# Performance work log

Hardware: AMD Instinct MI355X
Metric: run time of the kernel (lower is better)

## Reference

```python
import sys
import jax, jax.numpy as jnp
import numpy as np

sys.setrecursionlimit(100000)

MARGIN = 200.0
SAME_MARGIN = 0.0
REL_MARGIN = MARGIN - SAME_MARGIN  # margin - same_margin


def km_algorithm(mp):
    """Faithful numpy port of the repo's recursive Kuhn-Munkres (host-side,
    exactly mirroring the original CPU round-trip). mp: (n, n) float64.
    Returns transport plan T with T[link[y], y] = 1/n for matched pairs."""
    n = mp.shape[0]
    link = np.full(n, -1, dtype=np.int64)
    lx = mp.max(axis=1).astype(np.float64).copy()
    ly = np.zeros(n, dtype=np.float64)
    st = {}

    def dfs(x):
        st['visx'][x] = True
        for y in range(n):
            if st['visy'][y]:
                continue
            tmp = lx[x] + ly[y] - mp[x, y]
            if abs(tmp) < 1e-5:
                st['visy'][y] = True
                if link[y] == -1 or dfs(link[y]):
                    link[y] = x
                    return True
            elif st['sla'][y] + 1e-5 > tmp:
                st['sla'][y] = tmp
        return False

    for x in range(n):
        st['sla'] = np.full(n, 1e10, dtype=np.float64)
        while True:
            st['visx'] = np.zeros(n, dtype=bool)
            st['visy'] = np.zeros(n, dtype=bool)
            if dfs(x):
                break
            d = st['sla'][~st['visy']].min()
            lx[st['visx']] -= d
            ly[st['visy']] += d
            st['sla'][~st['visy']] -= d
    T = np.zeros((n, n), dtype=np.float64)
    for i in range(n):
        if link[i] != -1:
            T[link[i], i] = 1.0 / n
    return T


def sim_label(l1, l2):
    # (n, n) float: 1 where labels equal
    return (l1[:, None] == l2[None, :]).astype(jnp.float32)


def ground_metric(f1, f2, sim):
    # pairwise squared euclidean distances: ||a||^2 - 2 a.b + ||b||^2
    sq1 = jnp.sum(f1 * f1, axis=1)[:, None]
    sq2 = jnp.sum(f2 * f2, axis=1)[None, :]
    d2 = sq1 - 2.0 * (f1 @ f2.T) + sq2
    hinge_gm = jnp.maximum(0.0, SAME_MARGIN + REL_MARGIN - d2)   # negative pairs
    same_gm = jnp.maximum(0.0, d2 - SAME_MARGIN)                 # positive pairs
    return sim * same_gm + (1.0 - sim) * hinge_gm                # mode='both'


def setup_inputs() -> dict:
    key = jax.random.key(0)
    k1, k2, k3, k4 = jax.random.split(key, 4)
    n, d = 128, 8192
    return {
        "inputs_batch1": jax.random.normal(k1, (n, d), dtype=jnp.float32),
        "inputs_batch2": jax.random.normal(k2, (n, d), dtype=jnp.float32),
        "targets_batch1": jax.random.randint(k3, (n,), 0, 16, dtype=jnp.int64) if jax.config.jax_enable_x64 else jax.random.randint(k3, (n,), 0, 16).astype(jnp.int32),
        "targets_batch2": jax.random.randint(k4, (n,), 0, 16, dtype=jnp.int64) if jax.config.jax_enable_x64 else jax.random.randint(k4, (n,), 0, 16).astype(jnp.int32),
    }


def reference(inputs_batch1, inputs_batch2, targets_batch1, targets_batch2):
    sim = sim_label(targets_batch1, targets_batch2)
    GM = ground_metric(inputs_batch1, inputs_batch2, sim)
    # host round-trip for KM assignment, as in the original module
    T = km_algorithm(np.asarray(jax.device_get(GM), dtype=np.float64))
    T = jnp.asarray(T, dtype=jnp.float32)
    loss = jnp.sum(GM * T)
    return loss
```

## Files before the change

kernel.cpp:

```cpp
#include <hip/hip_runtime.h>

#define N 128
#define DIM 8192
#define NN (N * N)
#define ZSPLIT 64
#define NW 16
#define GSTRIDE 130
#define NSTR 65

__device__ __forceinline__ void wave_fence() {
    __threadfence_block();
    __builtin_amdgcn_wave_barrier();
}
__device__ __forceinline__ double embed_key(double v, int j) {
    long long b = __double_as_longlong(v);
    return __longlong_as_double((b & ~127LL) | (long long)j);
}

__global__ __launch_bounds__(256) void d2_partial(const float* __restrict__ A,
                                                  const float* __restrict__ B,
                                                  float* __restrict__ d2p,
                                                  float* __restrict__ sqAp,
                                                  float* __restrict__ sqBp) {
    __shared__ float As[32][68];
    __shared__ float Bk[64][36];
    const int tid = threadIdx.x;
    const int bi = blockIdx.x, bj = blockIdx.y, bz = blockIdx.z;
    const int tx = tid & 15, ty = tid >> 4;
    const int row0 = bi * 32, col0 = bj * 32;
    const int kbase = bz * 128;

    if (bj == 0) {
        const int r = tid >> 3, seg = tid & 7;
        const float* pa = &A[(row0 + r) * DIM + kbase + seg * 16];
        float s = 0.f;
        #pragma unroll
        for (int u = 0; u < 4; ++u) {
            float4 v = *(const float4*)&pa[u * 4];
            s = fmaf(v.x, v.x, fmaf(v.y, v.y, fmaf(v.z, v.z, fmaf(v.w, v.w, s))));
        }
        #pragma unroll
        for (int o = 1; o < 8; o <<= 1) s += __shfl_xor(s, o, 64);
        if (seg == 0) sqAp[bz * 128 + row0 + r] = s;
    }
    if (bi == 0) {
        const int r = tid >> 3, seg = tid & 7;
        const float* pb = &B[(col0 + r) * DIM + kbase + seg * 16];
        float s = 0.f;
        #pragma unroll
        for (int u = 0; u < 4; ++u) {
            float4 v = *(const float4*)&pb[u * 4];
            s = fmaf(v.x, v.x, fmaf(v.y, v.y, fmaf(v.z, v.z, fmaf(v.w, v.w, s))));
        }
        #pragma unroll
        for (int o = 1; o < 8; o <<= 1) s += __shfl_xor(s, o, 64);
        if (seg == 0) sqBp[bz * 128 + col0 + r] = s;
    }

    float a00 = 0.f, a01 = 0.f, a10 = 0.f, a11 = 0.f;
    for (int it = 0; it < 2; ++it) {
        const int k0 = kbase + it * 64;
        __syncthreads();
        #pragma unroll
        for (int s = 0; s < 2; ++s) {
            int e = tid + s * 256;
            int r = e >> 4, q = e & 15;
            *(float4*)&As[r][q * 4] = *(const float4*)&A[(row0 + r) * DIM + k0 + q * 4];
        }
        #pragma unroll
        for (int s = 0; s < 2; ++s) {
            int r = tid & 31;
            int kq = (tid >> 5) + s * 8;
            float4 b4 = *(const float4*)&B[(col0 + r) * DIM + k0 + kq * 4];
            Bk[kq * 4 + 0][r] = b4.x;
            Bk[kq * 4 + 1][r] = b4.y;
            Bk[kq * 4 + 2][r] = b4.z;
            Bk[kq * 4 + 3][r] = b4.w;
        }
        __syncthreads();
        #pragma unroll
        for (int kk = 0; kk < 64; kk += 4) {
            float x0[4], x1[4];
            *(float4*)x0 = *(const float4*)&As[2 * ty][kk];
            *(float4*)x1 = *(const float4*)&As[2 * ty + 1][kk];
            float y[4][2];
            #pragma unroll
            for (int q = 0; q < 4; ++q)
                *(float2*)y[q] = *(const float2*)&Bk[kk + q][2 * tx];
            #pragma unroll
            for (int q = 0; q < 4; ++q) {
                a00 = fmaf(x0[q], y[q][0], a00);
                a01 = fmaf(x0[q], y[q][1], a01);
                a10 = fmaf(x1[q], y[q][0], a10);
                a11 = fmaf(x1[q], y[q][1], a11);
            }
        }
    }
    const int o0 = (row0 + 2 * ty) * N + col0 + 2 * tx;
    float* dst = d2p + bz * NN;
    *(float2*)&dst[o0]     = make_float2(a00, a01);
    *(float2*)&dst[o0 + N] = make_float2(a10, a11);
}

__global__ __launch_bounds__(256) void reduce_gm(const float* __restrict__ d2p,
                                                 const float* __restrict__ sqAp,
                                                 const float* __restrict__ sqBp,
                                                 const int* __restrict__ t1,
                                                 const int* __restrict__ t2,
                                                 float* __restrict__ gm,
                                                 int* __restrict__ flagarr) {
    __shared__ float sqA_l[128], sqB_l[128];
    __shared__ int bf;
    const int tid = threadIdx.x;
    if (tid == 0) bf = 0;
    {
        const int c = tid & 127;
        const float* src = (tid < 128) ? (sqBp + c) : (sqAp + c);
        float t0 = 0.f, t1_ = 0.f, t2_ = 0.f, t3 = 0.f, t4 = 0.f, t5 = 0.f, t6 = 0.f, t7 = 0.f;
        #pragma unroll
        for (int z = 0; z < ZSPLIT; z += 8) {
            t0 += src[(z + 0) * 128]; t1_ += src[(z + 1) * 128];
            t2_ += src[(z + 2) * 128]; t3 += src[(z + 3) * 128];
            t4 += src[(z + 4) * 128]; t5 += src[(z + 5) * 128];
            t6 += src[(z + 6) * 128]; t7 += src[(z + 7) * 128];
        }
        float s = ((t0 + t1_) + (t2_ + t3)) + ((t4 + t5) + (t6 + t7));
        if (tid < 128) sqB_l[c] = s; else sqA_l[c] = s;
    }
    const int o = blockIdx.x * 256 + tid;
    float s0 = 0.f, s1 = 0.f, s2 = 0.f, s3 = 0.f, s4 = 0.f, s5 = 0.f, s6 = 0.f, s7 = 0.f;
    const float* p = d2p + o;
    #pragma unroll
    for (int z = 0; z < ZSPLIT; z += 8) {
        s0 += p[(z + 0) * NN]; s1 += p[(z + 1) * NN];
        s2 += p[(z + 2) * NN]; s3 += p[(z + 3) * NN];
        s4 += p[(z + 4) * NN]; s5 += p[(z + 5) * NN];
        s6 += p[(z + 6) * NN]; s7 += p[(z + 7) * NN];
    }
    float dot = ((s0 + s1) + (s2 + s3)) + ((s4 + s5) + (s6 + s7));
    __syncthreads();
    const int i = o >> 7, j = o & 127;
    const float s = sqA_l[i] + sqB_l[j] - 2.f * dot;
    const int l1 = t1[i], l2 = t2[j];
    const bool same = (l1 == l2);
    float g = same ? fmaxf(s, 0.f) : fmaxf(200.f - s, 0.f);
    gm[o] = g;
    bool bad = (!same && g > 0.f) || l1 < 0 || l1 > 63 || l2 < 0 || l2 > 63;
    unsigned long long m = __ballot(bad);
    if ((tid & 63) == 0 && m) atomicOr(&bf, 1);
    __syncthreads();
    if (tid == 0) flagarr[blockIdx.x] = bf;
}

__global__ __launch_bounds__(64) void solve_classes(const float* __restrict__ gm,
                                                    const int* __restrict__ flagarr,
                                                    const int* __restrict__ t1,
                                                    const int* __restrict__ t2,
                                                    double* __restrict__ cls_val) {
    __shared__ float ncls[64 * NSTR];
    __shared__ int rowl[64], coll[64];
    __shared__ int rcnt[64], ccnt[64];
    __shared__ int tasks[64];
    __shared__ int clm[64];

    const int lane = threadIdx.x;
    const int l1a = t1[lane] & 63, l1b = t1[lane + 64] & 63;
    const int l2a = t2[lane] & 63, l2b = t2[lane + 64] & 63;
    const int fl  = flagarr[lane];
    rcnt[lane] = 0; ccnt[lane] = 0;
    __syncthreads();
    atomicAdd(&rcnt[l1a], 1); atomicAdd(&rcnt[l1b], 1);
    atomicAdd(&ccnt[l2a], 1); atomicAdd(&ccnt[l2b], 1);
    __syncthreads();
    const bool flag = (__ballot(fl != 0) != 0ull);
    int ntasks;
    {
        int R = rcnt[lane], C = ccnt[lane];
        bool small = (!flag) && (R > 0) && (C > 0) && (R <= 64) && (C <= 64);
        unsigned long long ms = __ballot(small);
        if (small) tasks[__popcll(ms & ((1ull << lane) - 1))] = lane;
        ntasks = (int)__popcll(ms);
    }
    __syncthreads();
    if ((int)blockIdx.x >= ntasks) {
        if (lane == 0) cls_val[blockIdx.x] = 0.0;
        return;
    }
    const int c = tasks[blockIdx.x];

    const unsigned long long mlt = (1ull << lane) - 1;
    unsigned long long b1 = __ballot(l1a == c);
    unsigned long long b2 = __ballot(l1b == c);
    if (l1a == c) rowl[__popcll(b1 & mlt)] = lane;
    if (l1b == c) rowl[__popcll(b1) + __popcll(b2 & mlt)] = lane + 64;
    const int Rn = (int)(__popcll(b1) + __popcll(b2));
    unsigned long long c1 = __ballot(l2a == c);
    unsigned long long c2 = __ballot(l2b == c);
    if (l2a == c) coll[__popcll(c1 & mlt)] = lane;
    if (l2b == c) coll[__popcll(c1) + __popcll(c2 & mlt)] = lane + 64;
    const int Cn = (int)(__popcll(c1) + __popcll(c2));
    __syncthreads();

    const bool T  = (Rn > Cn);
    const int n_  = T ? Cn : Rn;
    const int m_  = T ? Rn : Cn;
    const int tot = n_ * m_;
    for (int e = lane; e < tot; e += 64) {
        int i = e / m_, j = e - i * m_;
        int gr = T ? rowl[j] : rowl[i];
        int gc = T ? coll[i] : coll[j];
        ncls[i * NSTR + j] = gm[gr * N + gc];
    }
    __syncthreads();

    const int W = (m_ <= 16) ? 16 : (m_ <= 32 ? 32 : 64);
    const bool cA = (lane < m_), rA = (lane < n_);

    double u = 0.0;
    if (rA) {
        float mx = 0.f;
        const float* row = &ncls[lane * NSTR];
        for (int j = 0; j < m_; ++j) mx = fmaxf(mx, row[j]);
        u = -(double)mx;
    }
    double v = 1e30;
    for (int i = 0; i < n_; ++i) {
        double ui = __shfl(u, i, 64);
        if (cA) v = fmin(v, -(double)ncls[i * NSTR + lane] - ui);
    }
    if (cA) clm[lane] = 0x7fffffff;
    wave_fence();
    int jc = -1;
    for (int j = 0; j < m_; ++j) {
        double vj = __shfl(v, j, 64);
        if (rA && jc < 0) {
            double s = -(double)ncls[lane * NSTR + j] - u - vj;
            if (s < 1e-7) jc = j;
        }
    }
    if (rA && jc >= 0) atomicMin(&clm[jc], lane);
    wave_fence();
    int p = -1;
    if (cA && clm[lane] != 0x7fffffff) p = clm[lane];
    bool rowm = (rA && jc >= 0 && clm[jc] == lane);

    for (int ir = 0; ir < n_; ++ir) {
        if (__shfl(rowm ? 1 : 0, ir, 64)) continue;
        double minv = 1e30, markD = -1.0, ent = -1.0;
        bool used = false; int way = -2;
        if (rA && lane == ir) ent = 0.0;
        double D = 0.0;
        int i0 = ir, jprev = -1;
        int guard = 2 * m_ + 8;
        while (guard-- > 0) {
            double ui = __shfl(u, i0, 64);
            if (cA && !used) {
                double cand = D - ui - (double)ncls[i0 * NSTR + lane] - v;
                if (cand < minv) { minv = cand; way = jprev; }
            }
            double kd = (cA && !used) ? embed_key(minv, lane) : 1e30;
            for (int o = 1; o < W; o <<= 1) kd = fmin(kd, __shfl_xor(kd, o, 64));
            long long kb = __double_as_longlong(kd);
            int j1 = (int)(kb & 127);
            double Dn = __longlong_as_double(kb & ~127LL);
            if (Dn > 1e29) break;
            D = Dn;
            int i1 = __shfl(p, j1, 64);
            if (i1 < 0) {
                int jj = j1;
                while (true) {
                    int wp = __shfl(way, jj, 64);
                    int pn = (wp < 0) ? ir : __shfl(p, wp, 64);
                    if (cA && lane == jj) p = pn;
                    if (wp < 0) break;
                    jj = wp;
                }
                if (rA && lane == ir) rowm = true;
                break;
            }
            if (cA && lane == j1) { used = true; markD = D; }
            if (rA && lane == i1) ent = D;
            jprev = j1; i0 = i1;
        }
        if (rA && ent   >= 0.0) u += D - ent;
        if (cA && markD >= 0.0) v -= D - markD;
    }

    double val = 0.0;
    if (cA && p >= 0) val = (double)ncls[p * NSTR + lane];
    #pragma unroll
    for (int o = 1; o < 64; o <<= 1) val += __shfl_xor(val, o, 64);
    if (lane == 0) cls_val[blockIdx.x] = val;
}

__global__ __launch_bounds__(1024) void finalize_kernel(const float* __restrict__ gm,
                                                        const int* __restrict__ flagarr,
                                                        const int* __restrict__ t1,
                                                        const int* __restrict__ t2,
                                                        const double* __restrict__ cls_val,
                                                        float* __restrict__ out) {
    __shared__ float gml[N * GSTRIDE];
    __shared__ int lbl1[N], lbl2[N];
    __shared__ int rowlist[N], collist[N];
    __shared__ int rcnt[64], ccnt[64], rstart[65], cstart[65], rcur[64], ccur[64];
    __shared__ int bigtasks[65];
    __shared__ int nbig_s, flag_s;
    __shared__ double ub[N + 1], vbp[N + 1], minvb[N + 1];
    __shared__ int pb[N + 1], wayb[N + 1], usedb[N + 1];
    __shared__ double redv[NW];
    __shared__ int redi[NW];
    __shared__ double big_total, small_sum;
    __shared__ int jfin_s;

    const int tid = threadIdx.x;
    if (tid < 64) { rcnt[tid] = 0; ccnt[tid] = 0; rcur[tid] = 0; ccur[tid] = 0; }
    if (tid == 0) { nbig_s = 0; flag_s = 0; big_total = 0.0; }
    if (tid < N)  { lbl1[tid] = t1[tid]; lbl2[tid] = t2[tid]; }
    __syncthreads();
    if (tid < 64 && flagarr[tid]) atomicOr(&flag_s, 1);
    if (tid < N) {
        atomicAdd(&rcnt[lbl1[tid] & 63], 1);
        atomicAdd(&ccnt[lbl2[tid] & 63], 1);
    }
    double sv = (tid < 64) ? cls_val[tid] : 0.0;
    __syncthreads();
    if (tid < 64) {
        int rs_ = rcnt[tid], cs_ = ccnt[tid];
        #pragma unroll
        for (int o = 1; o < 64; o <<= 1) {
            int tr = __shfl_up(rs_, o, 64);
            int tc = __shfl_up(cs_, o, 64);
            if (tid >= o) { rs_ += tr; cs_ += tc; }
        }
        rstart[tid + 1] = rs_;
        cstart[tid + 1] = cs_;
        if (tid == 0) { rstart[0] = 0; cstart[0] = 0; }
        if (!flag_s) {
            int R = rcnt[tid], C = ccnt[tid];
            bool big = (R > 0) && (C > 0) && ((R > 64) || (C > 64));
            unsigned long long mb = __ballot(big);
            if (big) bigtasks[__popcll(mb & ((1ull << tid) - 1))] = tid;
            if (tid == 0) nbig_s = __popcll(mb);
        } else if (tid == 0) { nbig_s = 1; bigtasks[0] = -1; }
        if (flag_s) sv = 0.0;
        #pragma unroll
        for (int o = 1; o < 64; o <<= 1) sv += __shfl_xor(sv, o, 64);
        if (tid == 0) small_sum = sv;
    }
    __syncthreads();

    const int nbig = nbig_s;
    if (nbig > 0) {
        if (tid < N) {
            int l1 = lbl1[tid] & 63;
            int p = atomicAdd(&rcur[l1], 1);
            rowlist[rstart[l1] + p] = tid;
            int l2 = lbl2[tid] & 63;
            int q = atomicAdd(&ccur[l2], 1);
            collist[cstart[l2] + q] = tid;
        }
        __syncthreads();
        #pragma unroll
        for (int pch = 0; pch < 16; ++pch) {
            int e = tid + pch * 1024;
            int i = e >> 7, j = e & 127;
            gml[i * GSTRIDE + j] = gm[rowlist[i] * N + collist[j]];
        }
        __syncthreads();

        for (int bt = 0; bt < nbig; ++bt) {
            const int c = bigtasks[bt];
            int Rn, Cn, rs, cs;
            if (c < 0) { Rn = N; Cn = N; rs = 0; cs = 0; }
            else { Rn = rcnt[c]; Cn = ccnt[c]; rs = rstart[c]; cs = cstart[c]; }
            const bool T = (Rn > Cn);
            const int n_ = T ? Cn : Rn, m_ = T ? Rn : Cn;
            const int rstep = T ? 1 : GSTRIDE;
            const int cstep = T ? GSTRIDE : 1;
            const int rb00 = T ? cs : rs * GSTRIDE;
            const int ob00 = T ? rs * GSTRIDE : cs;
            auto cost = [&](int i, int j) -> double {
                return -(double)gml[rb00 + i * rstep + ob00 + j * cstep];
            };
            for (int x = tid; x <= m_; x += 1024) { vbp[x] = 0.0; pb[x] = 0; }
            for (int x = tid; x <= n_; x += 1024) { ub[x] = 0.0; }
            __syncthreads();
            for (int i = 1; i <= n_; ++i) {
                if (tid == 0) pb[0] = i;
                for (int x = tid; x <= m_; x += 1024) { minvb[x] = 1e300; usedb[x] = 0; }
                __syncthreads();
                int j0 = 0;
                int guard = 2 * m_ + 8;
                while (guard-- > 0) {
                    if (tid == 0) usedb[j0] = 1;
                    __syncthreads();
                    const int i0 = pb[j0];
                    double dl = 1e300; int jl = 0;
                    if (tid < m_) {
                        int j = tid + 1;
                        if (!usedb[j]) {
                            double cur = cost(i0 - 1, j - 1) - ub[i0] - vbp[j];
                            if (cur < minvb[j]) { minvb[j] = cur; wayb[j] = j0; }
                            dl = minvb[j]; jl = j;
                        }
                    }
                    double rv = dl; int ri = jl;
                    #pragma unroll
                    for (int o = 32; o > 0; o >>= 1) {
                        double ov = __shfl_down(rv, o, 64);
                        int oi2 = __shfl_down(ri, o, 64);
                        if (ov < rv) { rv = ov; ri = oi2; }
                    }
                    if ((tid & 63) == 0) { redv[tid >> 6] = rv; redi[tid >> 6] = ri; }
                    __syncthreads();
                    if (tid == 0) {
                        double bd = 1e300; int bj = 0;
                        for (int q = 0; q < NW; ++q) if (redv[q] < bd) { bd = redv[q]; bj = redi[q]; }
                        redv[0] = bd; redi[0] = bj;
                    }
                    __syncthreads();
                    const double delta = redv[0];
                    const int j1 = redi[0];
                    if (tid < m_) {
                        int j = tid + 1;
                        if (usedb[j]) { ub[pb[j]] += delta; vbp[j] -= delta; }
                        else          { minvb[j] -= delta; }
                    }
                    if (tid == 0) ub[pb[0]] += delta;
                    __syncthreads();
                    j0 = j1;
                    if (pb[j0] == 0) break;
                }
                if (tid == 0) jfin_s = j0;
                __syncthreads();
                if (tid == 0) {
                    int jj = jfin_s;
                    while (jj) { int jp = wayb[jj]; pb[jj] = pb[jp]; jj = jp; }
                }
                __syncthreads();
            }
            double bl = 0.0;
            if (tid < m_) { int j = tid + 1; if (pb[j] != 0) bl = -cost(pb[j] - 1, j - 1); }
            #pragma unroll
            for (int o = 32; o > 0; o >>= 1) bl += __shfl_down(bl, o, 64);
            if ((tid & 63) == 0) redv[tid >> 6] = bl;
            __syncthreads();
            if (tid == 0) { double s = 0; for (int q = 0; q < NW; ++q) s += redv[q]; big_total += s; }
            __syncthreads();
        }
    }

    if (tid == 0) out[0] = (float)((small_sum + big_total) / (double)N);
}

extern "C" void kernel_launch(void* const* d_in, const int* in_sizes, int n_in,
                              void* d_out, int out_size, void* d_ws, size_t ws_size,
                              hipStream_t stream) {
    const float* A  = (const float*)d_in[0];
    const float* B  = (const float*)d_in[1];
    const int*   t1 = (const int*)d_in[2];
    const int*   t2 = (const int*)d_in[3];
    float* out = (float*)d_out;
    float* d2p = (float*)d_ws;
    float* gm  = d2p + ZSPLIT * NN;
    int*   flagarr = (int*)(gm + NN);
    double* cls_val = (double*)(flagarr + 64);
    float* sqAp = (float*)(cls_val + 64);
    float* sqBp = sqAp + ZSPLIT * 128;

    d2_partial<<<dim3(4, 4, ZSPLIT), 256, 0, stream>>>(A, B, d2p, sqAp, sqBp);
    reduce_gm<<<64, 256, 0, stream>>>(d2p, sqAp, sqBp, t1, t2, gm, flagarr);
    solve_classes<<<64, 64, 0, stream>>>(gm, flagarr, t1, t2, cls_val);
    finalize_kernel<<<1, 1024, 0, stream>>>(gm, flagarr, t1, t2, cls_val, out);
}
```

Before: 91.13 us.

## Fuse reduce and per-class assignment kernels, halve K-split of distance GEMM

Merges the partial-sum reduction kernel and the per-class Hungarian solver into one kernel, so one launch disappears. Each block recomputes its class's cost submatrix directly from the partial dot products instead of reading the global GM written by another block. The GEMM K-split is halved (32 slices of 256), which halves the partial buffer that must be reduced but gives fewer blocks of parallelism. The per-class solver no longer checks the global bad-pair flag, so it always solves classes and relies on the finalize kernel to handle the flagged case.

New measurement: 93.17 us. 1.02x slower.

```diff
diff --git a/kernel.cpp b/kernel.cpp
--- a/kernel.cpp
+++ b/kernel.cpp
@@ -3,7 +3,7 @@
 #define N 128
 #define DIM 8192
 #define NN (N * N)
-#define ZSPLIT 64
+#define ZSPLIT 32
 #define NW 16
 #define GSTRIDE 130
 #define NSTR 65
@@ -28,14 +28,14 @@
     const int bi = blockIdx.x, bj = blockIdx.y, bz = blockIdx.z;
     const int tx = tid & 15, ty = tid >> 4;
     const int row0 = bi * 32, col0 = bj * 32;
-    const int kbase = bz * 128;
+    const int kbase = bz * 256;
 
     if (bj == 0) {
         const int r = tid >> 3, seg = tid & 7;
-        const float* pa = &A[(row0 + r) * DIM + kbase + seg * 16];
+        const float* pa = &A[(row0 + r) * DIM + kbase + seg * 32];
         float s = 0.f;
         #pragma unroll
-        for (int u = 0; u < 4; ++u) {
+        for (int u = 0; u < 8; ++u) {
             float4 v = *(const float4*)&pa[u * 4];
             s = fmaf(v.x, v.x, fmaf(v.y, v.y, fmaf(v.z, v.z, fmaf(v.w, v.w, s))));
         }
@@ -45,10 +45,10 @@
     }
     if (bi == 0) {
         const int r = tid >> 3, seg = tid & 7;
-        const float* pb = &B[(col0 + r) * DIM + kbase + seg * 16];
+        const float* pb = &B[(col0 + r) * DIM + kbase + seg * 32];
         float s = 0.f;
         #pragma unroll
-        for (int u = 0; u < 4; ++u) {
+        for (int u = 0; u < 8; ++u) {
             float4 v = *(const float4*)&pb[u * 4];
             s = fmaf(v.x, v.x, fmaf(v.y, v.y, fmaf(v.z, v.z, fmaf(v.w, v.w, s))));
         }
@@ -58,7 +58,7 @@
     }
 
     float a00 = 0.f, a01 = 0.f, a10 = 0.f, a11 = 0.f;
-    for (int it = 0; it < 2; ++it) {
+    for (int it = 0; it < 4; ++it) {
         const int k0 = kbase + it * 64;
         __syncthreads();
         #pragma unroll
@@ -102,16 +102,23 @@
     *(float2*)&dst[o0 + N] = make_float2(a10, a11);
 }
 
-__global__ __launch_bounds__(256) void reduce_gm(const float* __restrict__ d2p,
-                                                 const float* __restrict__ sqAp,
-                                                 const float* __restrict__ sqBp,
-                                                 const int* __restrict__ t1,
-                                                 const int* __restrict__ t2,
-                                                 float* __restrict__ gm,
-                                                 int* __restrict__ flagarr) {
+__global__ __launch_bounds__(256) void reduce_solve(const float* __restrict__ d2p,
+                                                    const float* __restrict__ sqAp,
+                                                    const float* __restrict__ sqBp,
+                                                    const int* __restrict__ t1,
+                                                    const int* __restrict__ t2,
+                                                    float* __restrict__ gm,
+                                                    int* __restrict__ flagarr,
+                                                    double* __restrict__ cls_val) {
+    __shared__ float ncls[64 * NSTR];
     __shared__ float sqA_l[128], sqB_l[128];
     __shared__ int bf;
+    __shared__ int rowl[64], coll[64], rcnt[64], ccnt[64], tasks64[64], clm[64];
+    __shared__ int sT, sn, sm, shave;
+
     const int tid = threadIdx.x;
+    const int blk = blockIdx.x;
+
     if (tid == 0) bf = 0;
     {
         const int c = tid & 127;
@@ -127,170 +134,187 @@
         float s = ((t0 + t1_) + (t2_ + t3)) + ((t4 + t5) + (t6 + t7));
         if (tid < 128) sqB_l[c] = s; else sqA_l[c] = s;
     }
-    const int o = blockIdx.x * 256 + tid;
-    float s0 = 0.f, s1 = 0.f, s2 = 0.f, s3 = 0.f, s4 = 0.f, s5 = 0.f, s6 = 0.f, s7 = 0.f;
-    const float* p = d2p + o;
-    #pragma unroll
-    for (int z = 0; z < ZSPLIT; z += 8) {
-        s0 += p[(z + 0) * NN]; s1 += p[(z + 1) * NN];
-        s2 += p[(z + 2) * NN]; s3 += p[(z + 3) * NN];
-        s4 += p[(z + 4) * NN]; s5 += p[(z + 5) * NN];
-        s6 += p[(z + 6) * NN]; s7 += p[(z + 7) * NN];
-    }
-    float dot = ((s0 + s1) + (s2 + s3)) + ((s4 + s5) + (s6 + s7));
-    __syncthreads();
-    const int i = o >> 7, j = o & 127;
-    const float s = sqA_l[i] + sqB_l[j] - 2.f * dot;
-    const int l1 = t1[i], l2 = t2[j];
-    const bool same = (l1 == l2);
-    float g = same ? fmaxf(s, 0.f) : fmaxf(200.f - s, 0.f);
-    gm[o] = g;
-    bool bad = (!same && g > 0.f) || l1 < 0 || l1 > 63 || l2 < 0 || l2 > 63;
-    unsigned long long m = __ballot(bad);
-    if ((tid & 63) == 0 && m) atomicOr(&bf, 1);
-    __syncthreads();
-    if (tid == 0) flagarr[blockIdx.x] = bf;
-}
-
-__global__ __launch_bounds__(64) void solve_classes(const float* __restrict__ gm,
-                                                    const int* __restrict__ flagarr,
-                                                    const int* __restrict__ t1,
-                                                    const int* __restrict__ t2,
-                                                    double* __restrict__ cls_val) {
-    __shared__ float ncls[64 * NSTR];
-    __shared__ int rowl[64], coll[64];
-    __shared__ int rcnt[64], ccnt[64];
-    __shared__ int tasks[64];
-    __shared__ int clm[64];
-
-    const int lane = threadIdx.x;
-    const int l1a = t1[lane] & 63, l1b = t1[lane + 64] & 63;
-    const int l2a = t2[lane] & 63, l2b = t2[lane + 64] & 63;
-    const int fl  = flagarr[lane];
-    rcnt[lane] = 0; ccnt[lane] = 0;
-    __syncthreads();
-    atomicAdd(&rcnt[l1a], 1); atomicAdd(&rcnt[l1b], 1);
-    atomicAdd(&ccnt[l2a], 1); atomicAdd(&ccnt[l2b], 1);
-    __syncthreads();
-    const bool flag = (__ballot(fl != 0) != 0ull);
-    int ntasks;
+    const int o = blk * 256 + tid;
+    float dot;
     {
-        int R = rcnt[lane], C = ccnt[lane];
-        bool small = (!flag) && (R > 0) && (C > 0) && (R <= 64) && (C <= 64);
-        unsigned long long ms = __ballot(small);
-        if (small) tasks[__popcll(ms & ((1ull << lane) - 1))] = lane;
-        ntasks = (int)__popcll(ms);
-    }
-    __syncthreads();
-    if ((int)blockIdx.x >= ntasks) {
-        if (lane == 0) cls_val[blockIdx.x] = 0.0;
+        const float* p = d2p + o;
+        float s0 = 0.f, s1 = 0.f, s2 = 0.f, s3 = 0.f, s4 = 0.f, s5 = 0.f, s6 = 0.f, s7 = 0.f;
+        #pragma unroll
+        for (int z = 0; z < ZSPLIT; z += 8) {
+            s0 += p[(z + 0) * NN]; s1 += p[(z + 1) * NN];
+            s2 += p[(z + 2) * NN]; s3 += p[(z + 3) * NN];
+            s4 += p[(z + 4) * NN]; s5 += p[(z + 5) * NN];
+            s6 += p[(z + 6) * NN]; s7 += p[(z + 7) * NN];
+        }
+        dot = ((s0 + s1) + (s2 + s3)) + ((s4 + s5) + (s6 + s7));
+    }
+    __syncthreads();
+    {
+        const int i = o >> 7, j = o & 127;
+        const float s = sqA_l[i] + sqB_l[j] - 2.f * dot;
+        const int l1 = t1[i], l2 = t2[j];
+        const bool same = (l1 == l2);
+        float g = same ? fmaxf(s, 0.f) : fmaxf(200.f - s, 0.f);
+        gm[o] = g;
+        bool bad = (!same && g > 0.f) || l1 < 0 || l1 > 63 || l2 < 0 || l2 > 63;
+        unsigned long long m = __ballot(bad);
+        if ((tid & 63) == 0 && m) atomicOr(&bf, 1);
+    }
+    __syncthreads();
+    if (tid == 0) flagarr[blk] = bf;
+
+    if (tid < 64) {
+        const int lane = tid;
+        const int l1a = t1[lane] & 63, l1b = t1[lane + 64] & 63;
+        const int l2a = t2[lane] & 63, l2b = t2[lane + 64] & 63;
+        rcnt[lane] = 0; ccnt[lane] = 0;
+        wave_fence();
+        atomicAdd(&rcnt[l1a], 1); atomicAdd(&rcnt[l1b], 1);
+        atomicAdd(&ccnt[l2a], 1); atomicAdd(&ccnt[l2b], 1);
+        wave_fence();
+        int ntasks;
+        {
+            int R = rcnt[lane], C = ccnt[lane];
+            bool small = (R > 0) && (C > 0) && (R <= 64) && (C <= 64);
+            unsigned long long ms = __ballot(small);
+            if (small) tasks64[__popcll(ms & ((1ull << lane) - 1))] = lane;
+            ntasks = (int)__popcll(ms);
+        }
+        wave_fence();
+        const bool have = (blk < ntasks);
+        if (have) {
+            const int c = tasks64[blk];
+            const unsigned long long mlt = (1ull << lane) - 1;
+            unsigned long long b1 = __ballot(l1a == c);
+            unsigned long long b2 = __ballot(l1b == c);
+            if (l1a == c) rowl[__popcll(b1 & mlt)] = lane;
+            if (l1b == c) rowl[__popcll(b1) + __popcll(b2 & mlt)] = lane + 64;
+            const int Rn = (int)(__popcll(b1) + __popcll(b2));
+            unsigned long long c1 = __ballot(l2a == c);
+            unsigned long long c2 = __ballot(l2b == c);
+            if (l2a == c) coll[__popcll(c1 & mlt)] = lane;
+            if (l2b == c) coll[__popcll(c1) + __popcll(c2 & mlt)] = lane + 64;
+            const int Cn = (int)(__popcll(c1) + __popcll(c2));
+            if (lane == 0) {
+                const bool T = (Rn > Cn);
+                sT = T ? 1 : 0;
+                sn = T ? Cn : Rn;
+                sm = T ? Rn : Cn;
+            }
+        }
+        if (lane == 0) shave = have ? 1 : 0;
+    }
+    __syncthreads();
+    if (!shave) {
+        if (tid == 0) cls_val[blk] = 0.0;
         return;
     }
-    const int c = tasks[blockIdx.x];
-
-    const unsigned long long mlt = (1ull << lane) - 1;
-    unsigned long long b1 = __ballot(l1a == c);
-    unsigned long long b2 = __ballot(l1b == c);
-    if (l1a == c) rowl[__popcll(b1 & mlt)] = lane;
-    if (l1b == c) rowl[__popcll(b1) + __popcll(b2 & mlt)] = lane + 64;
-    const int Rn = (int)(__popcll(b1) + __popcll(b2));
-    unsigned long long c1 = __ballot(l2a == c);
-    unsigned long long c2 = __ballot(l2b == c);
-    if (l2a == c) coll[__popcll(c1 & mlt)] = lane;
-    if (l2b == c) coll[__popcll(c1) + __popcll(c2 & mlt)] = lane + 64;
-    const int Cn = (int)(__popcll(c1) + __popcll(c2));
-    __syncthreads();
-
-    const bool T  = (Rn > Cn);
-    const int n_  = T ? Cn : Rn;
-    const int m_  = T ? Rn : Cn;
-    const int tot = n_ * m_;
-    for (int e = lane; e < tot; e += 64) {
-        int i = e / m_, j = e - i * m_;
-        int gr = T ? rowl[j] : rowl[i];
-        int gc = T ? coll[i] : coll[j];
-        ncls[i * NSTR + j] = gm[gr * N + gc];
-    }
-    __syncthreads();
-
-    const int W = (m_ <= 16) ? 16 : (m_ <= 32 ? 32 : 64);
-    const bool cA = (lane < m_), rA = (lane < n_);
-
-    double u = 0.0;
-    if (rA) {
-        float mx = 0.f;
-        const float* row = &ncls[lane * NSTR];
-        for (int j = 0; j < m_; ++j) mx = fmaxf(mx, row[j]);
-        u = -(double)mx;
-    }
-    double v = 1e30;
-    for (int i = 0; i < n_; ++i) {
-        double ui = __shfl(u, i, 64);
-        if (cA) v = fmin(v, -(double)ncls[i * NSTR + lane] - ui);
-    }
-    if (cA) clm[lane] = 0x7fffffff;
-    wave_fence();
-    int jc = -1;
-    for (int j = 0; j < m_; ++j) {
-        double vj = __shfl(v, j, 64);
-        if (rA && jc < 0) {
-            double s = -(double)ncls[lane * NSTR + j] - u - vj;
-            if (s < 1e-7) jc = j;
-        }
-    }
-    if (rA && jc >= 0) atomicMin(&clm[jc], lane);
-    wave_fence();
-    int p = -1;
-    if (cA && clm[lane] != 0x7fffffff) p = clm[lane];
-    bool rowm = (rA && jc >= 0 && clm[jc] == lane);
-
-    for (int ir = 0; ir < n_; ++ir) {
-        if (__shfl(rowm ? 1 : 0, ir, 64)) continue;
-        double minv = 1e30, markD = -1.0, ent = -1.0;
-        bool used = false; int way = -2;
-        if (rA && lane == ir) ent = 0.0;
-        double D = 0.0;
-        int i0 = ir, jprev = -1;
-        int guard = 2 * m_ + 8;
-        while (guard-- > 0) {
-            double ui = __shfl(u, i0, 64);
-            if (cA && !used) {
-                double cand = D - ui - (double)ncls[i0 * NSTR + lane] - v;
-                if (cand < minv) { minv = cand; way = jprev; }
-            }
-            double kd = (cA && !used) ? embed_key(minv, lane) : 1e30;
-            for (int o = 1; o < W; o <<= 1) kd = fmin(kd, __shfl_xor(kd, o, 64));
-            long long kb = __double_as_longlong(kd);
-            int j1 = (int)(kb & 127);
-            double Dn = __longlong_as_double(kb & ~127LL);
-            if (Dn > 1e29) break;
-            D = Dn;
-            int i1 = __shfl(p, j1, 64);
-            if (i1 < 0) {
-                int jj = j1;
-                while (true) {
-                    int wp = __shfl(way, jj, 64);
-                    int pn = (wp < 0) ? ir : __shfl(p, wp, 64);
-                    if (cA && lane == jj) p = pn;
-                    if (wp < 0) break;
-                    jj = wp;
+
+    {
+        const int n_ = sn, m_ = sm, T = sT;
+        const int tot = n_ * m_;
+        const int sub = tid & 3;
+        for (int e = tid >> 2; e < tot; e += 64) {
+            const int i = e / m_, j = e - i * m_;
+            const int gr = T ? rowl[j] : rowl[i];
+            const int gc = T ? coll[i] : coll[j];
+            const float* p = d2p + gr * N + gc + sub * 8 * NN;
+            float q0 = 0.f, q1 = 0.f, q2 = 0.f, q3 = 0.f;
+            #pragma unroll
+            for (int z = 0; z < 8; z += 4) {
+                q0 += p[(z + 0) * NN]; q1 += p[(z + 1) * NN];
+                q2 += p[(z + 2) * NN]; q3 += p[(z + 3) * NN];
+            }
+            float s = (q0 + q1) + (q2 + q3);
+            s += __shfl_xor(s, 1, 64);
+            s += __shfl_xor(s, 2, 64);
+            if (sub == 0)
+                ncls[i * NSTR + j] = fmaxf(sqA_l[gr] + sqB_l[gc] - 2.f * s, 0.f);
+        }
+    }
+    __syncthreads();
+
+    double val = 0.0;
+    if (tid < 64) {
+        const int lane = tid;
+        const int n_ = sn, m_ = sm;
+        const int W = (m_ <= 16) ? 16 : (m_ <= 32 ? 32 : 64);
+        const bool cA = (lane < m_), rA = (lane < n_);
+
+        double u = 0.0;
+        if (rA) {
+            float mx = 0.f;
+            const float* row = &ncls[lane * NSTR];
+            for (int j = 0; j < m_; ++j) mx = fmaxf(mx, row[j]);
+            u = -(double)mx;
+        }
+        double v = 1e30;
+        for (int i = 0; i < n_; ++i) {
+            double ui = __shfl(u, i, 64);
+            if (cA) v = fmin(v, -(double)ncls[i * NSTR + lane] - ui);
+        }
+        if (cA) clm[lane] = 0x7fffffff;
+        wave_fence();
+        int jc = -1;
+        for (int j = 0; j < m_; ++j) {
+            double vj = __shfl(v, j, 64);
+            if (rA && jc < 0) {
+                double s = -(double)ncls[lane * NSTR + j] - u - vj;
+                if (s < 1e-7) jc = j;
+            }
+        }
+        if (rA && jc >= 0) atomicMin(&clm[jc], lane);
+        wave_fence();
+        int p = -1;
+        if (cA && clm[lane] != 0x7fffffff) p = clm[lane];
+        bool rowm = (rA && jc >= 0 && clm[jc] == lane);
+
+        for (int ir = 0; ir < n_; ++ir) {
+            if (__shfl(rowm ? 1 : 0, ir, 64)) continue;
+            double minv = 1e30, markD = -1.0, ent = -1.0;
+            bool used = false; int way = -2;
+            if (rA && lane == ir) ent = 0.0;
+            double D = 0.0;
+            int i0 = ir, jprev = -1;
+            int guard = 2 * m_ + 8;
+            while (guard-- > 0) {
+                double ui = __shfl(u, i0, 64);
+                if (cA && !used) {
+                    double cand = D - ui - (double)ncls[i0 * NSTR + lane] - v;
+                    if (cand < minv) { minv = cand; way = jprev; }
                 }
-                if (rA && lane == ir) rowm = true;
-                break;
-            }
-            if (cA && lane == j1) { used = true; markD = D; }
-            if (rA && lane == i1) ent = D;
-            jprev = j1; i0 = i1;
-        }
-        if (rA && ent   >= 0.0) u += D - ent;
-        if (cA && markD >= 0.0) v -= D - markD;
-    }
-
-    double val = 0.0;
-    if (cA && p >= 0) val = (double)ncls[p * NSTR + lane];
-    #pragma unroll
-    for (int o = 1; o < 64; o <<= 1) val += __shfl_xor(val, o, 64);
-    if (lane == 0) cls_val[blockIdx.x] = val;
+                double kd = (cA && !used) ? embed_key(minv, lane) : 1e30;
+                for (int oo = 1; oo < W; oo <<= 1) kd = fmin(kd, __shfl_xor(kd, oo, 64));
+                long long kb = __double_as_longlong(kd);
+                int j1 = (int)(kb & 127);
+                double Dn = __longlong_as_double(kb & ~127LL);
+                if (Dn > 1e29) break;
+                D = Dn;
+                int i1 = __shfl(p, j1, 64);
+                if (i1 < 0) {
+                    int jj = j1;
+                    while (true) {
+                        int wp = __shfl(way, jj, 64);
+                        int pn = (wp < 0) ? ir : __shfl(p, wp, 64);
+                        if (cA && lane == jj) p = pn;
+                        if (wp < 0) break;
+                        jj = wp;
+                    }
+                    if (rA && lane == ir) rowm = true;
+                    break;
+                }
+                if (cA && lane == j1) { used = true; markD = D; }
+                if (rA && lane == i1) ent = D;
+                jprev = j1; i0 = i1;
+            }
+            if (rA && ent   >= 0.0) u += D - ent;
+            if (cA && markD >= 0.0) v -= D - markD;
+        }
+        if (cA && p >= 0) val = (double)ncls[p * NSTR + lane];
+        #pragma unroll
+        for (int oo = 1; oo < 64; oo <<= 1) val += __shfl_xor(val, oo, 64);
+    }
+    if (tid == 0) cls_val[blk] = val;
 }
 
 __global__ __launch_bounds__(1024) void finalize_kernel(const float* __restrict__ gm,
@@ -469,7 +493,6 @@
     float* sqBp = sqAp + ZSPLIT * 128;
 
     d2_partial<<<dim3(4, 4, ZSPLIT), 256, 0, stream>>>(A, B, d2p, sqAp, sqBp);
-    reduce_gm<<<64, 256, 0, stream>>>(d2p, sqAp, sqBp, t1, t2, gm, flagarr);
-    solve_classes<<<64, 64, 0, stream>>>(gm, flagarr, t1, t2, cls_val);
+    reduce_solve<<<64, 256, 0, stream>>>(d2p, sqAp, sqBp, t1, t2, gm, flagarr, cls_val);
     finalize_kernel<<<1, 1024, 0, stream>>>(gm, flagarr, t1, t2, cls_val, out);
 }
```
